# Optimization experiments

Hardware: AMD Instinct MI355X
Metric: run time of the kernel (lower is better)

The kernel has to match this reference:

```python
import jax, jax.numpy as jnp
import numpy as np

EMBED_DIM = 1024
NUM_HEADS = 16
HEAD_DIM = EMBED_DIM // NUM_HEADS
SEG_LEN = 1024  # all segment_lengths equal, dilation_rate == 1


def setup_inputs() -> dict:
    key = jax.random.key(0)
    k1, k2, k3 = jax.random.split(key, 3)
    B, S, E = 2, 4096, EMBED_DIM
    x = jax.random.normal(k1, (B, S, E), dtype=jnp.float32)
    w_qkv = jax.random.normal(k2, (3 * E, E), dtype=jnp.float32) * (E ** -0.5)
    b_qkv = jnp.zeros((3 * E,), dtype=jnp.float32)
    w_out = jax.random.normal(k3, (E, E), dtype=jnp.float32) * (E ** -0.5)
    b_out = jnp.zeros((E,), dtype=jnp.float32)
    return {"x": x, "w_qkv": w_qkv, "b_qkv": b_qkv, "w_out": w_out, "b_out": b_out}


def reference(x, w_qkv, b_qkv, w_out, b_out):
    B, S, E = x.shape
    H, Dh = NUM_HEADS, HEAD_DIM
    scale = 1.0 / np.sqrt(Dh).astype(np.float32)
    # QKV projection
    qkv = x @ w_qkv.T + b_qkv                      # [B, S, 3E]
    qkv = qkv.reshape(B, S, 3, H, Dh).transpose(2, 0, 3, 1, 4)  # [3, B, H, S, Dh]
    q, k, v = qkv[0], qkv[1], qkv[2]
    # Segments tile the sequence; each query attends only within its segment
    # (block-diagonal attention; online-softmax combine across segments is
    # trivial since the segments are disjoint in the query dimension).
    n = S // SEG_LEN
    q = q.reshape(B, H, n, SEG_LEN, Dh)
    k = k.reshape(B, H, n, SEG_LEN, Dh)
    v = v.reshape(B, H, n, SEG_LEN, Dh)
    scores = jnp.einsum("bhnqd,bhnkd->bhnqk", q, k) * scale
    attn = jax.nn.softmax(scores, axis=-1)
    out = jnp.einsum("bhnqk,bhnkd->bhnqd", attn, v)  # [B, H, n, seg, Dh]
    out = out.reshape(B, H, S, Dh).transpose(0, 2, 1, 3).reshape(B, S, E)
    return out @ w_out.T + b_out
```

## Files before the change

kernel.cpp:

```cpp
#include <hip/hip_runtime.h>

typedef __bf16 bf16x8 __attribute__((ext_vector_type(8)));
typedef float f32x4 __attribute__((ext_vector_type(4)));

#define SL2E 0.18033688011112042f

__device__ __forceinline__ unsigned short f2bf(float f) {
  union { float f; unsigned u; } v; v.f = f;
  unsigned r = v.u + 0x7fffu + ((v.u >> 16) & 1u);
  return (unsigned short)(r >> 16);
}

__device__ __forceinline__ float fast_exp2(float x) {
#if __has_builtin(__builtin_amdgcn_exp2f)
  return __builtin_amdgcn_exp2f(x);
#else
  return exp2f(x);
#endif
}

__device__ __forceinline__ unsigned pack_bf2(float lo, float hi) {
  union { float f; unsigned u; } a, b;
  a.f = lo; b.f = hi;
#if __has_builtin(__builtin_amdgcn_perm)
  return __builtin_amdgcn_perm(b.u + 0x7fffu, a.u + 0x7fffu, 0x07060302u);
#else
  return ((b.u + 0x7fffu) & 0xffff0000u) | ((a.u + 0x7fffu) >> 16);
#endif
}

__device__ __forceinline__ void gload16(const unsigned short* g, unsigned short* l) {
  __builtin_amdgcn_global_load_lds(
      (const __attribute__((address_space(1))) unsigned int*)g,
      (__attribute__((address_space(3))) unsigned int*)l, 16, 0, 0);
}

__global__ __launch_bounds__(256) void f32_to_bf16_all(
    const float* __restrict__ x, const float* __restrict__ wq, const float* __restrict__ wo,
    unsigned short* __restrict__ xb, unsigned short* __restrict__ wqb, unsigned short* __restrict__ wob) {
  int i = blockIdx.x * 256 + threadIdx.x;
  const float* src; unsigned short* dst; int off;
  if (i < 2097152) { src = x; dst = xb; off = i; }
  else if (i < 2883584) { src = wq; dst = wqb; off = i - 2097152; }
  else if (i < 3145728) { src = wo; dst = wob; off = i - 2883584; }
  else return;
  float4 v = ((const float4*)src)[off];
  ushort4 o;
  o.x = f2bf(v.x); o.y = f2bf(v.y); o.z = f2bf(v.z); o.w = f2bf(v.w);
  ((ushort4*)dst)[off] = o;
}


__global__ __launch_bounds__(256) void gemm_qkv(
    const unsigned short* __restrict__ A,
    const unsigned short* __restrict__ Bt,
    const float* __restrict__ bias,
    unsigned short* __restrict__ Qb,
    unsigned short* __restrict__ Kb,
    unsigned short* __restrict__ Vtb) {
  const int K = 1024;
  __shared__ unsigned short As[128 * 64];
  __shared__ unsigned short Bs[128 * 64];
  int tid = threadIdx.x;
  int m0 = blockIdx.x * 128, n0 = blockIdx.y * 128;
  int w = tid >> 6, lane = tid & 63, l15 = lane & 15, quad = lane >> 4;
  int wm = (w & 1) * 64, wn = (w >> 1) * 64;

  f32x4 acc[4][4] = {};

  int rs = w * 32 + (lane >> 3);
  int cs = ((lane & 7) ^ (lane >> 3)) * 8;
  const unsigned short* Ag = A + (m0 + rs) * K + cs;
  const unsigned short* Bg = Bt + (n0 + rs) * K + cs;
  unsigned short* Asl = As + w * 2048;
  unsigned short* Bsl = Bs + w * 2048;

  for (int kt = 0; kt < K; kt += 64) {
    __syncthreads();
#pragma unroll
    for (int i = 0; i < 4; ++i) {
      gload16(Ag + i * 8 * K + kt, Asl + i * 512);
      gload16(Bg + i * 8 * K + kt, Bsl + i * 512);
    }
    __syncthreads();
#pragma unroll
    for (int kk = 0; kk < 2; ++kk) {
      int swk = (((kk * 4 + quad) ^ (l15 & 7))) * 8;
      bf16x8 af[4], bfr[4];
#pragma unroll
      for (int i = 0; i < 4; ++i) af[i] = *(const bf16x8*)(As + (wm + i * 16 + l15) * 64 + swk);
#pragma unroll
      for (int j = 0; j < 4; ++j) bfr[j] = *(const bf16x8*)(Bs + (wn + j * 16 + l15) * 64 + swk);
#pragma unroll
      for (int i = 0; i < 4; ++i)
#pragma unroll
        for (int j = 0; j < 4; ++j)
          acc[i][j] = __builtin_amdgcn_mfma_f32_16x16x32_bf16(af[i], bfr[j], acc[i][j], 0, 0, 0);
    }
  }

  int b = m0 >> 12;
  int sblk = (m0 & 4095) + wm + quad * 4;
#pragma unroll
  for (int j = 0; j < 4; ++j) {
    int n_j = n0 + wn + j * 16 + l15;
    float bv = bias[n_j];
    int t = n_j >> 10, h = (n_j >> 6) & 15, d = n_j & 63;
    if (t == 2) {
      int vbase = ((b * 16 + h) * 64 + d) * 4096;
#pragma unroll
      for (int i = 0; i < 4; ++i) {
        int s = sblk + i * 16;
        ushort4 pk;
        pk.x = f2bf(acc[i][j][0] + bv);
        pk.y = f2bf(acc[i][j][1] + bv);
        pk.z = f2bf(acc[i][j][2] + bv);
        pk.w = f2bf(acc[i][j][3] + bv);
        *(ushort4*)(Vtb + vbase + s) = pk;
      }
    } else {
      unsigned short* dst = (t == 0) ? Qb : Kb;
      float sc = (t == 0) ? SL2E : 1.0f;
      int base = (b * 16 + h) * 4096 * 64 + d;
#pragma unroll
      for (int i = 0; i < 4; ++i)
#pragma unroll
        for (int r = 0; r < 4; ++r) {
          int s = sblk + i * 16 + r;
          dst[base + s * 64] = f2bf((acc[i][j][r] + bv) * sc);
        }
    }
  }
}

#define LDP 72
#define SWZ(r, cg) ((((r) * 8) + ((cg) ^ ((r) & 7))) * 8)

__global__ __launch_bounds__(256) void attn_k(
    const unsigned short* __restrict__ Qb,
    const unsigned short* __restrict__ Kb,
    const unsigned short* __restrict__ Vtb,
    unsigned short* __restrict__ Ab) {
  __shared__ unsigned short KV[2][2][4096];
  __shared__ unsigned short Ps[4][16 * LDP];

  int tid = threadIdx.x;
  int idx = blockIdx.x;
  int grp = idx & 127, qblk = idx >> 7;
  int seg = grp & 3, h = (grp >> 2) & 15, b = grp >> 6;
  int w = tid >> 6, lane = tid & 63, l15 = lane & 15, quad = lane >> 4;
  int bh = b * 16 + h;
  int q0 = seg * 1024 + qblk * 256 + w * 64;

  const unsigned short* Kg = Kb + (bh * 4096 + seg * 1024) * 64;
  const unsigned short* Vg = Vtb + bh * 64 * 4096 + seg * 1024;

  int r0 = w * 16 + (lane >> 3);
  int cs = ((lane & 7) ^ (lane >> 3)) * 8;

  const unsigned short* Qg = Qb + (bh * 4096 + q0) * 64;
  bf16x8 qf[4][2];
#pragma unroll
  for (int qb = 0; qb < 4; ++qb)
#pragma unroll
    for (int kk = 0; kk < 2; ++kk)
      qf[qb][kk] = *(const bf16x8*)(Qg + (qb * 16 + l15) * 64 + kk * 32 + quad * 8);

  f32x4 o[4][4] = {};
  float lsum[4] = {0.f, 0.f, 0.f, 0.f};
  unsigned short* Pw = Ps[w];

  {
    unsigned short* dk = &KV[0][0][w * 1024];
    unsigned short* dv = &KV[0][1][w * 1024];
    gload16(Kg + r0 * 64 + cs, dk);
    gload16(Kg + (r0 + 8) * 64 + cs, dk + 512);
    gload16(Vg + r0 * 4096 + cs, dv);
    gload16(Vg + (r0 + 8) * 4096 + cs, dv + 512);
  }

#pragma unroll 2
  for (int kt = 0; kt < 16; ++kt) {
    int cur = kt & 1;
    __syncthreads();
    if (kt < 15) {
      unsigned short* dk = &KV[cur ^ 1][0][w * 1024];
      unsigned short* dv = &KV[cur ^ 1][1][w * 1024];
      const unsigned short* kN = Kg + (kt + 1) * 4096;
      const unsigned short* vN = Vg + (kt + 1) * 64;
      gload16(kN + r0 * 64 + cs, dk);
      gload16(kN + (r0 + 8) * 64 + cs, dk + 512);
      gload16(vN + r0 * 4096 + cs, dv);
      gload16(vN + (r0 + 8) * 4096 + cs, dv + 512);
    }
    const unsigned short* Kt = KV[cur][0];
    const unsigned short* Vt = KV[cur][1];

    uint2 pp[4][4];
#pragma unroll
    for (int half = 0; half < 2; ++half) {
      f32x4 st[2][4] = {};
#pragma unroll
      for (int kk = 0; kk < 2; ++kk) {
        int cg = kk * 4 + quad;
        bf16x8 kf0 = *(const bf16x8*)(Kt + SWZ(half * 32 + l15, cg));
        bf16x8 kf1 = *(const bf16x8*)(Kt + SWZ(half * 32 + 16 + l15, cg));
#pragma unroll
        for (int qb = 0; qb < 4; ++qb) {
          st[0][qb] = __builtin_amdgcn_mfma_f32_16x16x32_bf16(kf0, qf[qb][kk], st[0][qb], 0, 0, 0);
          st[1][qb] = __builtin_amdgcn_mfma_f32_16x16x32_bf16(kf1, qf[qb][kk], st[1][qb], 0, 0, 0);
        }
      }
#pragma unroll
      for (int kb = 0; kb < 2; ++kb)
#pragma unroll
        for (int qb = 0; qb < 4; ++qb) {
          f32x4 s = st[kb][qb];
          float p0 = fast_exp2(s[0]), p1 = fast_exp2(s[1]);
          float p2 = fast_exp2(s[2]), p3 = fast_exp2(s[3]);
          lsum[qb] += (p0 + p1) + (p2 + p3);
          uint2 d;
          d.x = pack_bf2(p0, p1);
          d.y = pack_bf2(p2, p3);
          pp[qb][half * 2 + kb] = d;
        }
    }

    bf16x8 vf[2][4];
#pragma unroll
    for (int kk = 0; kk < 2; ++kk)
#pragma unroll
      for (int db = 0; db < 4; ++db)
        vf[kk][db] = *(const bf16x8*)(Vt + SWZ(db * 16 + l15, kk * 4 + quad));
#pragma unroll
    for (int qb = 0; qb < 4; ++qb) {
#pragma unroll
      for (int g = 0; g < 4; ++g)
        *(uint2*)(Pw + l15 * LDP + g * 16 + quad * 4) = pp[qb][g];
#pragma unroll
      for (int kk = 0; kk < 2; ++kk) {
        bf16x8 pa = *(const bf16x8*)(Pw + l15 * LDP + kk * 32 + quad * 8);
#pragma unroll
        for (int db = 0; db < 4; ++db)
          o[qb][db] = __builtin_amdgcn_mfma_f32_16x16x32_bf16(pa, vf[kk][db], o[qb][db], 0, 0, 0);
      }
    }
  }

#pragma unroll
  for (int qb = 0; qb < 4; ++qb) {
    lsum[qb] += __shfl_xor(lsum[qb], 16);
    lsum[qb] += __shfl_xor(lsum[qb], 32);
  }

  float* Wf = (float*)(&KV[0][0][0]) + w * 1024;
#pragma unroll
  for (int qb = 0; qb < 4; ++qb) {
#pragma unroll
    for (int db = 0; db < 4; ++db)
#pragma unroll
      for (int r = 0; r < 4; ++r)
        Wf[(quad * 4 + r) * 64 + db * 16 + l15] = o[qb][db][r];
    float inv = 1.0f / lsum[qb];
    float4 x0 = *(float4*)(Wf + l15 * 64 + quad * 8);
    float4 x1 = *(float4*)(Wf + l15 * 64 + quad * 8 + 4);
    float4 x2 = *(float4*)(Wf + l15 * 64 + (quad + 4) * 8);
    float4 x3 = *(float4*)(Wf + l15 * 64 + (quad + 4) * 8 + 4);
    uint4 u0, u1;
    u0.x = pack_bf2(x0.x * inv, x0.y * inv);
    u0.y = pack_bf2(x0.z * inv, x0.w * inv);
    u0.z = pack_bf2(x1.x * inv, x1.y * inv);
    u0.w = pack_bf2(x1.z * inv, x1.w * inv);
    u1.x = pack_bf2(x2.x * inv, x2.y * inv);
    u1.y = pack_bf2(x2.z * inv, x2.w * inv);
    u1.z = pack_bf2(x3.x * inv, x3.y * inv);
    u1.w = pack_bf2(x3.z * inv, x3.w * inv);
    int sg = q0 + qb * 16 + l15;
    int base = (b * 4096 + sg) * 1024 + h * 64;
    *(uint4*)(Ab + base + quad * 8) = u0;
    *(uint4*)(Ab + base + (quad + 4) * 8) = u1;
  }
}

__global__ __launch_bounds__(256) void gemm_out(
    const unsigned short* __restrict__ A,
    const unsigned short* __restrict__ Bt,
    const float* __restrict__ bias,
    float* __restrict__ C) {
  const int K = 1024;
  __shared__ unsigned short As[128 * 64];
  __shared__ unsigned short Bs[128 * 64];
  int tid = threadIdx.x;
  int m0 = blockIdx.x * 128, n0 = blockIdx.y * 128;
  int w = tid >> 6, lane = tid & 63, l15 = lane & 15, quad = lane >> 4;
  int wm = (w & 1) * 64, wn = (w >> 1) * 64;

  f32x4 acc[4][4] = {};

  int rs = w * 32 + (lane >> 3);
  int cs = ((lane & 7) ^ (lane >> 3)) * 8;
  const unsigned short* Ag = A + (m0 + rs) * K + cs;
  const unsigned short* Bg = Bt + (n0 + rs) * K + cs;
  unsigned short* Asl = As + w * 2048;
  unsigned short* Bsl = Bs + w * 2048;

  for (int kt = 0; kt < K; kt += 64) {
    __syncthreads();
#pragma unroll
    for (int i = 0; i < 4; ++i) {
      gload16(Ag + i * 8 * K + kt, Asl + i * 512);
      gload16(Bg + i * 8 * K + kt, Bsl + i * 512);
    }
    __syncthreads();
#pragma unroll
    for (int kk = 0; kk < 2; ++kk) {
      int swk = (((kk * 4 + quad) ^ (l15 & 7))) * 8;
      bf16x8 af[4], bfr[4];
#pragma unroll
      for (int i = 0; i < 4; ++i) af[i] = *(const bf16x8*)(As + (wm + i * 16 + l15) * 64 + swk);
#pragma unroll
      for (int j = 0; j < 4; ++j) bfr[j] = *(const bf16x8*)(Bs + (wn + j * 16 + l15) * 64 + swk);
#pragma unroll
      for (int i = 0; i < 4; ++i)
#pragma unroll
        for (int j = 0; j < 4; ++j)
          acc[i][j] = __builtin_amdgcn_mfma_f32_16x16x32_bf16(af[i], bfr[j], acc[i][j], 0, 0, 0);
    }
  }

#pragma unroll
  for (int j = 0; j < 4; ++j) {
    int n_j = n0 + wn + j * 16 + l15;
    float bv = bias[n_j];
#pragma unroll
    for (int i = 0; i < 4; ++i)
#pragma unroll
      for (int r = 0; r < 4; ++r) {
        int m = m0 + wm + i * 16 + quad * 4 + r;
        C[m * 1024 + n_j] = acc[i][j][r] + bv;
      }
  }
}

extern "C" void kernel_launch(void* const* d_in, const int* in_sizes, int n_in,
                              void* d_out, int out_size, void* d_ws, size_t ws_size,
                              hipStream_t stream) {
  const float* x     = (const float*)d_in[0];
  const float* w_qkv = (const float*)d_in[1];
  const float* b_qkv = (const float*)d_in[2];
  const float* w_out = (const float*)d_in[3];
  const float* b_out = (const float*)d_in[4];
  float* out = (float*)d_out;
  char* ws = (char*)d_ws;

  unsigned short* wqkvb = (unsigned short*)(ws);
  unsigned short* woutb = (unsigned short*)(ws + 6291456);
  unsigned short* Qb    = (unsigned short*)(ws + 8388608);
  unsigned short* Kb    = (unsigned short*)(ws + 25165824);
  unsigned short* Vtb   = (unsigned short*)(ws + 41943040);
  unsigned short* xb    = (unsigned short*)(ws + 58720256);
  unsigned short* Ab    = xb;

  f32_to_bf16_all<<<12288, 256, 0, stream>>>(x, w_qkv, w_out, xb, wqkvb, woutb);
  gemm_qkv<<<dim3(64, 24), 256, 0, stream>>>(xb, wqkvb, b_qkv, Qb, Kb, Vtb);
  attn_k<<<512, 256, 0, stream>>>(Qb, Kb, Vtb, Ab);
  gemm_out<<<dim3(64, 8), 256, 0, stream>>>(Ab, woutb, b_out, out);
}
```

Before: 228.8 us.

## Double-buffer LDS tiles in QKV and output GEMMs to overlap loads with MFMA

Both projection GEMMs now use two LDS buffers per operand. The next K-tile's global-to-LDS loads are issued while MFMAs run on the current tile, and each iteration needs one barrier instead of two. The K loop is unrolled by two through a macro so buffer indices are compile-time constants. The aim is to hide global load latency behind compute, at the cost of doubling LDS per block, which can lower occupancy.

Result: slower. 238.5 us (+4.2%).

```diff
diff --git a/kernel.cpp b/kernel.cpp
--- a/kernel.cpp
+++ b/kernel.cpp
@@ -51,6 +51,34 @@
 }
 
 
+#define GEMM_K_BODY(CUR, KT)                                                  \
+  {                                                                           \
+    __syncthreads();                                                          \
+    if ((KT) < 15) {                                                          \
+      const int off = ((KT) + 1) * 64;                                        \
+      unsigned short* Ad = &As[(CUR) ^ 1][w * 2048];                          \
+      unsigned short* Bd = &Bs[(CUR) ^ 1][w * 2048];                          \
+      _Pragma("unroll") for (int i = 0; i < 4; ++i) {                         \
+        gload16(Ag + i * 8 * K + off, Ad + i * 512);                          \
+        gload16(Bg + i * 8 * K + off, Bd + i * 512);                          \
+      }                                                                       \
+    }                                                                         \
+    const unsigned short* Ac = As[CUR];                                       \
+    const unsigned short* Bc = Bs[CUR];                                       \
+    _Pragma("unroll") for (int kk = 0; kk < 2; ++kk) {                        \
+      int swk = (((kk * 4 + quad) ^ (l15 & 7))) * 8;                          \
+      bf16x8 af[4], bfr[4];                                                   \
+      _Pragma("unroll") for (int i = 0; i < 4; ++i)                           \
+        af[i] = *(const bf16x8*)(Ac + (wm + i * 16 + l15) * 64 + swk);        \
+      _Pragma("unroll") for (int j = 0; j < 4; ++j)                           \
+        bfr[j] = *(const bf16x8*)(Bc + (wn + j * 16 + l15) * 64 + swk);       \
+      _Pragma("unroll") for (int i = 0; i < 4; ++i)                           \
+        _Pragma("unroll") for (int j = 0; j < 4; ++j)                         \
+          acc[i][j] = __builtin_amdgcn_mfma_f32_16x16x32_bf16(                \
+              af[i], bfr[j], acc[i][j], 0, 0, 0);                             \
+    }                                                                         \
+  }
+
 __global__ __launch_bounds__(256) void gemm_qkv(
     const unsigned short* __restrict__ A,
     const unsigned short* __restrict__ Bt,
@@ -59,8 +87,8 @@
     unsigned short* __restrict__ Kb,
     unsigned short* __restrict__ Vtb) {
   const int K = 1024;
-  __shared__ unsigned short As[128 * 64];
-  __shared__ unsigned short Bs[128 * 64];
+  __shared__ unsigned short As[2][128 * 64];
+  __shared__ unsigned short Bs[2][128 * 64];
   int tid = threadIdx.x;
   int m0 = blockIdx.x * 128, n0 = blockIdx.y * 128;
   int w = tid >> 6, lane = tid & 63, l15 = lane & 15, quad = lane >> 4;
@@ -72,31 +100,16 @@
   int cs = ((lane & 7) ^ (lane >> 3)) * 8;
   const unsigned short* Ag = A + (m0 + rs) * K + cs;
   const unsigned short* Bg = Bt + (n0 + rs) * K + cs;
-  unsigned short* Asl = As + w * 2048;
-  unsigned short* Bsl = Bs + w * 2048;
-
-  for (int kt = 0; kt < K; kt += 64) {
-    __syncthreads();
-#pragma unroll
-    for (int i = 0; i < 4; ++i) {
-      gload16(Ag + i * 8 * K + kt, Asl + i * 512);
-      gload16(Bg + i * 8 * K + kt, Bsl + i * 512);
-    }
-    __syncthreads();
-#pragma unroll
-    for (int kk = 0; kk < 2; ++kk) {
-      int swk = (((kk * 4 + quad) ^ (l15 & 7))) * 8;
-      bf16x8 af[4], bfr[4];
-#pragma unroll
-      for (int i = 0; i < 4; ++i) af[i] = *(const bf16x8*)(As + (wm + i * 16 + l15) * 64 + swk);
-#pragma unroll
-      for (int j = 0; j < 4; ++j) bfr[j] = *(const bf16x8*)(Bs + (wn + j * 16 + l15) * 64 + swk);
-#pragma unroll
-      for (int i = 0; i < 4; ++i)
-#pragma unroll
-        for (int j = 0; j < 4; ++j)
-          acc[i][j] = __builtin_amdgcn_mfma_f32_16x16x32_bf16(af[i], bfr[j], acc[i][j], 0, 0, 0);
-    }
+
+#pragma unroll
+  for (int i = 0; i < 4; ++i) {
+    gload16(Ag + i * 8 * K, &As[0][w * 2048] + i * 512);
+    gload16(Bg + i * 8 * K, &Bs[0][w * 2048] + i * 512);
+  }
+
+  for (int kt2 = 0; kt2 < 8; ++kt2) {
+    GEMM_K_BODY(0, 2 * kt2)
+    GEMM_K_BODY(1, 2 * kt2 + 1)
   }
 
   int b = m0 >> 12;
@@ -288,8 +301,8 @@
     const float* __restrict__ bias,
     float* __restrict__ C) {
   const int K = 1024;
-  __shared__ unsigned short As[128 * 64];
-  __shared__ unsigned short Bs[128 * 64];
+  __shared__ unsigned short As[2][128 * 64];
+  __shared__ unsigned short Bs[2][128 * 64];
   int tid = threadIdx.x;
   int m0 = blockIdx.x * 128, n0 = blockIdx.y * 128;
   int w = tid >> 6, lane = tid & 63, l15 = lane & 15, quad = lane >> 4;
@@ -301,31 +314,16 @@
   int cs = ((lane & 7) ^ (lane >> 3)) * 8;
   const unsigned short* Ag = A + (m0 + rs) * K + cs;
   const unsigned short* Bg = Bt + (n0 + rs) * K + cs;
-  unsigned short* Asl = As + w * 2048;
-  unsigned short* Bsl = Bs + w * 2048;
-
-  for (int kt = 0; kt < K; kt += 64) {
-    __syncthreads();
-#pragma unroll
-    for (int i = 0; i < 4; ++i) {
-      gload16(Ag + i * 8 * K + kt, Asl + i * 512);
-      gload16(Bg + i * 8 * K + kt, Bsl + i * 512);
-    }
-    __syncthreads();
-#pragma unroll
-    for (int kk = 0; kk < 2; ++kk) {
-      int swk = (((kk * 4 + quad) ^ (l15 & 7))) * 8;
-      bf16x8 af[4], bfr[4];
-#pragma unroll
-      for (int i = 0; i < 4; ++i) af[i] = *(const bf16x8*)(As + (wm + i * 16 + l15) * 64 + swk);
-#pragma unroll
-      for (int j = 0; j < 4; ++j) bfr[j] = *(const bf16x8*)(Bs + (wn + j * 16 + l15) * 64 + swk);
-#pragma unroll
-      for (int i = 0; i < 4; ++i)
-#pragma unroll
-        for (int j = 0; j < 4; ++j)
-          acc[i][j] = __builtin_amdgcn_mfma_f32_16x16x32_bf16(af[i], bfr[j], acc[i][j], 0, 0, 0);
-    }
+
+#pragma unroll
+  for (int i = 0; i < 4; ++i) {
+    gload16(Ag + i * 8 * K, &As[0][w * 2048] + i * 512);
+    gload16(Bg + i * 8 * K, &Bs[0][w * 2048] + i * 512);
+  }
+
+  for (int kt2 = 0; kt2 < 8; ++kt2) {
+    GEMM_K_BODY(0, 2 * kt2)
+    GEMM_K_BODY(1, 2 * kt2 + 1)
   }
 
 #pragma unroll
```
